# Kernel optimization log

Hardware: AMD Instinct MI355X
Metric: run time of the kernel (lower is better)

The kernel has to match this reference:

```python
import jax, jax.numpy as jnp
import numpy as np

B, LQ, LK, DK, DV = 16, 1024, 1024, 256, 256
NEG = -1e9


def setup_inputs() -> dict:
    key = jax.random.key(0)
    kq, kk, kv, kw, km = jax.random.split(key, 5)
    return {
        "query": jax.random.normal(kq, (B, LQ, DK), dtype=jnp.float32),
        "key": jax.random.normal(kk, (B, LK, DK), dtype=jnp.float32),
        "value": jax.random.normal(kv, (B, LK, DV), dtype=jnp.float32),
        "w": jax.random.normal(kw, (DK,), dtype=jnp.float32),  # Linear(d_k,1,bias=False) weight
        "mask": jax.random.randint(km, (B, LQ, LK), 0, 2, dtype=jnp.int32),
    }


def reference(query, key, value, w, mask):
    # Bahdanau additive score: alignment_layer(query[:, :, None] + key[:, None, :]).squeeze(-1)
    # Exact linear decomposition: W·(q+k) = W·q + W·k, avoiding the (Lq,Lk,d_k) intermediate.
    q_s = jnp.einsum("bqd,d->bq", query, w)  # [B, Lq]
    k_s = jnp.einsum("bkd,d->bk", key, w)    # [B, Lk]
    scores = q_s[:, :, None] + k_s[:, None, :]  # [B, Lq, Lk]
    scores = jnp.where(mask == 0, NEG, scores)
    p_attn = jax.nn.softmax(scores, axis=-1)
    return jnp.matmul(p_attn, value)  # [B, Lq, Dv]
```

## Files before the change

### kernel.cpp

```cpp
#include <hip/hip_runtime.h>
#include <math.h>


#define NB     16
#define NL     1024
#define ND     256
#define NBKT   128

__global__ __launch_bounds__(256)
void ksm_kernel(const float* __restrict__ key, const float* __restrict__ w,
                const int* __restrict__ mask,
                float* __restrict__ ks, unsigned short* __restrict__ bmtab) {
    int wid  = threadIdx.x >> 6;
    int lane = threadIdx.x & 63;
    int row  = blockIdx.x * 4 + wid;

    const float4* krow = (const float4*)(key + (size_t)row * ND);
    float4 kv = krow[lane];
    float4 wv = ((const float4*)w)[lane];
    const int4* mrow4 = (const int4*)(mask + (size_t)row * NL);
    int4 m0 = mrow4[lane], m1 = mrow4[lane + 64];
    int4 m2 = mrow4[lane + 128], m3 = mrow4[lane + 192];

    float p = kv.x * wv.x + kv.y * wv.y + kv.z * wv.z + kv.w * wv.w;
    #pragma unroll
    for (int off = 32; off > 0; off >>= 1)
        p += __shfl_xor(p, off, 64);

    unsigned int bits = 0;
    bits |= (m0.x != 0 ? 1u : 0u) << 0;  bits |= (m0.y != 0 ? 1u : 0u) << 1;
    bits |= (m0.z != 0 ? 1u : 0u) << 2;  bits |= (m0.w != 0 ? 1u : 0u) << 3;
    bits |= (m1.x != 0 ? 1u : 0u) << 4;  bits |= (m1.y != 0 ? 1u : 0u) << 5;
    bits |= (m1.z != 0 ? 1u : 0u) << 6;  bits |= (m1.w != 0 ? 1u : 0u) << 7;
    bits |= (m2.x != 0 ? 1u : 0u) << 8;  bits |= (m2.y != 0 ? 1u : 0u) << 9;
    bits |= (m2.z != 0 ? 1u : 0u) << 10; bits |= (m2.w != 0 ? 1u : 0u) << 11;
    bits |= (m3.x != 0 ? 1u : 0u) << 12; bits |= (m3.y != 0 ? 1u : 0u) << 13;
    bits |= (m3.z != 0 ? 1u : 0u) << 14; bits |= (m3.w != 0 ? 1u : 0u) << 15;

    bmtab[(size_t)row * 64 + lane] = (unsigned short)bits;
    if (lane == 0) ks[row] = p;
}

__global__ __launch_bounds__(512)
void attn_kernel(const float* __restrict__ value, const int* __restrict__ mask,
                 const float* __restrict__ ks,
                 const unsigned short* __restrict__ bmtab,
                 float* __restrict__ out) {
    __shared__ float  lds_V[64 * ND];
    __shared__ float2 pk_lds[NL];
    __shared__ int    cnt[NBKT];
    __shared__ int    cur[NBKT];
    __shared__ float  wred[8];
    __shared__ float  csum[16];

    const int t    = threadIdx.x;
    const int wid  = t >> 6;
    const int lane = t & 63;
    const int row0 = blockIdx.x * 32 + wid * 4;
    const int b    = row0 >> 10;

    const float4* vbase = (const float4*)(value + ((size_t)b << 10) * ND);
    const float*  ksb   = ks + b * NL;

    if (t < NBKT) cnt[t] = 0;

    float v0 = ksb[t], v1 = ksb[t + 512];

    float mx = fmaxf(v0, v1);
    #pragma unroll
    for (int off = 32; off > 0; off >>= 1)
        mx = fmaxf(mx, __shfl_xor(mx, off, 64));
    if (lane == 0) wred[wid] = mx;
    __syncthreads();
    float m = wred[0];
    #pragma unroll
    for (int j = 1; j < 8; ++j) m = fmaxf(m, wred[j]);

    float e0v = __expf(v0 - m), e1v = __expf(v1 - m);
    int b0 = (int)fminf(m - v0, (float)(NBKT - 1));
    int b1 = (int)fminf(m - v1, (float)(NBKT - 1));
    atomicAdd(&cnt[b0], 1); atomicAdd(&cnt[b1], 1);
    __syncthreads();

    if (wid == 0) {
        int a   = cnt[lane];
        int b2v = cnt[lane + 64];
        int sa = a, sb = b2v;
        #pragma unroll
        for (int d = 1; d < 64; d <<= 1) {
            int na = __shfl_up(sa, d, 64);
            int nb = __shfl_up(sb, d, 64);
            if (lane >= d) { sa += na; sb += nb; }
        }
        int tot = __shfl(sa, 63, 64);
        sb += tot;
        cur[lane]      = sa - a;
        cur[lane + 64] = sb - b2v;
    }
    __syncthreads();

    int p0i = atomicAdd(&cur[b0], 1);
    int p1i = atomicAdd(&cur[b1], 1);
    pk_lds[p0i] = make_float2(e0v, __int_as_float(t));
    pk_lds[p1i] = make_float2(e1v, __int_as_float(t + 512));
    __syncthreads();

    #pragma unroll
    for (int cc = 0; cc < 2; ++cc) {
        int chunk = wid * 2 + cc;
        float s = pk_lds[chunk * 64 + lane].x;
        #pragma unroll
        for (int off = 32; off > 0; off >>= 1)
            s += __shfl_xor(s, off, 64);
        if (lane == 0) csum[chunk] = s;
    }

    float2 p0 = pk_lds[lane];
    int   k0  = __float_as_int(p0.y);
    float e0  = p0.x;
    int   e0i = __float_as_int(e0);

    const int L     = (k0 >> 2) & 63;
    const int shift = (k0 & 3) + ((k0 >> 8) << 2);

    unsigned short t0 = bmtab[(size_t)(row0 + 0) * 64 + L];
    unsigned short t1 = bmtab[(size_t)(row0 + 1) * 64 + L];
    unsigned short t2 = bmtab[(size_t)(row0 + 2) * 64 + L];
    unsigned short t3 = bmtab[(size_t)(row0 + 3) * 64 + L];

    #pragma unroll
    for (int j = 0; j < 8; ++j) {
        int s   = wid * 8 + j;
        int ksr = __builtin_amdgcn_readlane(k0, s);
        ((float4*)lds_V)[s * 64 + lane] = vbase[(size_t)ksr * 64 + lane];
    }

    bool mb0 = (t0 >> shift) & 1;
    bool mb1 = (t1 >> shift) & 1;
    bool mb2 = (t2 >> shift) & 1;
    bool mb3 = (t3 >> shift) & 1;
    unsigned long long bm0 = __ballot(mb0);
    unsigned long long bm1 = __ballot(mb1);
    unsigned long long bm2 = __ballot(mb2);
    unsigned long long bm3 = __ballot(mb3);

    auto zsum = [&](bool mb) -> float {
        float wz = mb ? e0 : 0.0f;
        #pragma unroll
        for (int off = 32; off > 0; off >>= 1)
            wz += __shfl_xor(wz, off, 64);
        return wz;
    };
    float z0 = zsum(mb0), z1 = zsum(mb1), z2 = zsum(mb2), z3 = zsum(mb3);

    __syncthreads();

    float4 acc0 = make_float4(0.f, 0.f, 0.f, 0.f);
    float4 acc1 = make_float4(0.f, 0.f, 0.f, 0.f);
    float4 acc2 = make_float4(0.f, 0.f, 0.f, 0.f);
    float4 acc3 = make_float4(0.f, 0.f, 0.f, 0.f);

    #pragma unroll 16
    for (int i = 0; i < 64; ++i) {
        float4 v = ((const float4*)lds_V)[i * 64 + lane];
        float ei = __int_as_float(__builtin_amdgcn_readlane(e0i, i));
        float w0 = ((bm0 >> i) & 1ull) ? ei : 0.0f;
        float w1 = ((bm1 >> i) & 1ull) ? ei : 0.0f;
        float w2 = ((bm2 >> i) & 1ull) ? ei : 0.0f;
        float w3 = ((bm3 >> i) & 1ull) ? ei : 0.0f;
        acc0.x += w0 * v.x; acc0.y += w0 * v.y; acc0.z += w0 * v.z; acc0.w += w0 * v.w;
        acc1.x += w1 * v.x; acc1.y += w1 * v.y; acc1.z += w1 * v.z; acc1.w += w1 * v.w;
        acc2.x += w2 * v.x; acc2.y += w2 * v.y; acc2.z += w2 * v.z; acc2.w += w2 * v.w;
        acc3.x += w3 * v.x; acc3.y += w3 * v.y; acc3.z += w3 * v.z; acc3.w += w3 * v.w;
    }

    float remA = 0.0f;
    #pragma unroll
    for (int j = 1; j < 16; ++j) remA += csum[j];

    auto finish_row = [&](int r, float4 acc, float Z) {
        const int* mrow = mask + (size_t)(row0 + r) * NL;
        float rsuf = remA;
        bool done = (rsuf <= 1e-5f * Z);
        for (int c = 1; c < 16 && !done; ++c) {
            float2 p = pk_lds[c * 64 + lane];
            float e  = p.x;
            int   k  = __float_as_int(p.y);
            bool mb  = (mrow[k] != 0);
            float dz = mb ? e : 0.0f;
            #pragma unroll
            for (int off = 32; off > 0; off >>= 1)
                dz += __shfl_xor(dz, off, 64);
            unsigned long long bmx = __ballot(mb);
            int eI = __float_as_int(e);
            for (int i = 0; i < 64; ++i) {
                float ei = __int_as_float(__builtin_amdgcn_readlane(eI, i));
                int   ki = __builtin_amdgcn_readlane(k, i);
                float w  = ((bmx >> i) & 1ull) ? ei : 0.0f;
                float4 v = vbase[(size_t)ki * 64 + lane];
                acc.x += w * v.x; acc.y += w * v.y;
                acc.z += w * v.z; acc.w += w * v.w;
            }
            Z += dz;
            rsuf -= csum[c];
            done = (rsuf <= 1e-5f * Z);
        }
        float4* orow = (float4*)(out + (size_t)(row0 + r) * ND);
        if (Z > 0.0f) {
            float inv = 1.0f / Z;
            orow[lane] = make_float4(acc.x * inv, acc.y * inv,
                                     acc.z * inv, acc.w * inv);
        } else {
            float4 s = make_float4(0.f, 0.f, 0.f, 0.f);
            for (int k = 0; k < NL; ++k) {
                float4 v = vbase[(size_t)k * 64 + lane];
                s.x += v.x; s.y += v.y; s.z += v.z; s.w += v.w;
            }
            const float inv = 1.0f / (float)NL;
            orow[lane] = make_float4(s.x * inv, s.y * inv, s.z * inv, s.w * inv);
        }
    };
    finish_row(0, acc0, z0);
    finish_row(1, acc1, z1);
    finish_row(2, acc2, z2);
    finish_row(3, acc3, z3);
}

extern "C" void kernel_launch(void* const* d_in, const int* in_sizes, int n_in,
                              void* d_out, int out_size, void* d_ws, size_t ws_size,
                              hipStream_t stream) {
    const float* key   = (const float*)d_in[1];
    const float* value = (const float*)d_in[2];
    const float* w     = (const float*)d_in[3];
    const int*   mask  = (const int*)d_in[4];
    float*       outp  = (float*)d_out;

    float* ks = (float*)d_ws;
    unsigned short* bmtab =
        (unsigned short*)(ks + NB * NL);

    ksm_kernel <<<NB * NL / 4, 256, 0, stream>>>(key, w, mask, ks, bmtab);
    attn_kernel<<<NB * NL / 32, 512, 0, stream>>>(value, mask, ks, bmtab, outp);
}
```

Measured before the change: 158.0 us.

## Halve attention block size and stage only half the top V rows in LDS

Attention blocks shrink from 512 to 256 threads (16 rows per block, twice as many blocks), and each thread now handles four key scores in the max, bucket-sort and exp phase. LDS staging of the top-weighted V rows drops from 64 to 32, so the remaining 32 rows are read straight from global memory inside the accumulation loop. The smaller LDS footprint is meant to let more blocks fit per CU and raise occupancy. In exchange, the per-batch key-score sort is repeated across twice as many blocks, and global V gathers are added to the inner loop.

```diff
diff --git a/kernel.cpp b/kernel.cpp
--- a/kernel.cpp
+++ b/kernel.cpp
@@ -6,6 +6,7 @@
 #define NL     1024
 #define ND     256
 #define NBKT   128
+#define NSTAGE 32
 
 __global__ __launch_bounds__(256)
 void ksm_kernel(const float* __restrict__ key, const float* __restrict__ w,
@@ -41,22 +42,22 @@
     if (lane == 0) ks[row] = p;
 }
 
-__global__ __launch_bounds__(512)
+__global__ __launch_bounds__(256)
 void attn_kernel(const float* __restrict__ value, const int* __restrict__ mask,
                  const float* __restrict__ ks,
                  const unsigned short* __restrict__ bmtab,
                  float* __restrict__ out) {
-    __shared__ float  lds_V[64 * ND];
+    __shared__ float  lds_V[NSTAGE * ND];
     __shared__ float2 pk_lds[NL];
     __shared__ int    cnt[NBKT];
     __shared__ int    cur[NBKT];
-    __shared__ float  wred[8];
+    __shared__ float  wred[4];
     __shared__ float  csum[16];
 
     const int t    = threadIdx.x;
     const int wid  = t >> 6;
     const int lane = t & 63;
-    const int row0 = blockIdx.x * 32 + wid * 4;
+    const int row0 = blockIdx.x * 16 + wid * 4;
     const int b    = row0 >> 10;
 
     const float4* vbase = (const float4*)(value + ((size_t)b << 10) * ND);
@@ -64,22 +65,24 @@
 
     if (t < NBKT) cnt[t] = 0;
 
-    float v0 = ksb[t], v1 = ksb[t + 512];
-
-    float mx = fmaxf(v0, v1);
+    float v0 = ksb[t], v1 = ksb[t + 256], v2 = ksb[t + 512], v3 = ksb[t + 768];
+
+    float mx = fmaxf(fmaxf(v0, v1), fmaxf(v2, v3));
     #pragma unroll
     for (int off = 32; off > 0; off >>= 1)
         mx = fmaxf(mx, __shfl_xor(mx, off, 64));
     if (lane == 0) wred[wid] = mx;
     __syncthreads();
-    float m = wred[0];
-    #pragma unroll
-    for (int j = 1; j < 8; ++j) m = fmaxf(m, wred[j]);
+    const float m = fmaxf(fmaxf(wred[0], wred[1]), fmaxf(wred[2], wred[3]));
 
     float e0v = __expf(v0 - m), e1v = __expf(v1 - m);
+    float e2v = __expf(v2 - m), e3v = __expf(v3 - m);
     int b0 = (int)fminf(m - v0, (float)(NBKT - 1));
     int b1 = (int)fminf(m - v1, (float)(NBKT - 1));
+    int b2 = (int)fminf(m - v2, (float)(NBKT - 1));
+    int b3 = (int)fminf(m - v3, (float)(NBKT - 1));
     atomicAdd(&cnt[b0], 1); atomicAdd(&cnt[b1], 1);
+    atomicAdd(&cnt[b2], 1); atomicAdd(&cnt[b3], 1);
     __syncthreads();
 
     if (wid == 0) {
@@ -101,13 +104,17 @@
 
     int p0i = atomicAdd(&cur[b0], 1);
     int p1i = atomicAdd(&cur[b1], 1);
+    int p2i = atomicAdd(&cur[b2], 1);
+    int p3i = atomicAdd(&cur[b3], 1);
     pk_lds[p0i] = make_float2(e0v, __int_as_float(t));
-    pk_lds[p1i] = make_float2(e1v, __int_as_float(t + 512));
-    __syncthreads();
-
-    #pragma unroll
-    for (int cc = 0; cc < 2; ++cc) {
-        int chunk = wid * 2 + cc;
+    pk_lds[p1i] = make_float2(e1v, __int_as_float(t + 256));
+    pk_lds[p2i] = make_float2(e2v, __int_as_float(t + 512));
+    pk_lds[p3i] = make_float2(e3v, __int_as_float(t + 768));
+    __syncthreads();
+
+    #pragma unroll
+    for (int cc = 0; cc < 4; ++cc) {
+        int chunk = wid * 4 + cc;
         float s = pk_lds[chunk * 64 + lane].x;
         #pragma unroll
         for (int off = 32; off > 0; off >>= 1)
@@ -161,8 +168,22 @@
     float4 acc3 = make_float4(0.f, 0.f, 0.f, 0.f);
 
     #pragma unroll 16
-    for (int i = 0; i < 64; ++i) {
+    for (int i = 0; i < NSTAGE; ++i) {
         float4 v = ((const float4*)lds_V)[i * 64 + lane];
+        float ei = __int_as_float(__builtin_amdgcn_readlane(e0i, i));
+        float w0 = ((bm0 >> i) & 1ull) ? ei : 0.0f;
+        float w1 = ((bm1 >> i) & 1ull) ? ei : 0.0f;
+        float w2 = ((bm2 >> i) & 1ull) ? ei : 0.0f;
+        float w3 = ((bm3 >> i) & 1ull) ? ei : 0.0f;
+        acc0.x += w0 * v.x; acc0.y += w0 * v.y; acc0.z += w0 * v.z; acc0.w += w0 * v.w;
+        acc1.x += w1 * v.x; acc1.y += w1 * v.y; acc1.z += w1 * v.z; acc1.w += w1 * v.w;
+        acc2.x += w2 * v.x; acc2.y += w2 * v.y; acc2.z += w2 * v.z; acc2.w += w2 * v.w;
+        acc3.x += w3 * v.x; acc3.y += w3 * v.y; acc3.z += w3 * v.z; acc3.w += w3 * v.w;
+    }
+    #pragma unroll 8
+    for (int i = NSTAGE; i < 64; ++i) {
+        int ksr  = __builtin_amdgcn_readlane(k0, i);
+        float4 v = vbase[(size_t)ksr * 64 + lane];
         float ei = __int_as_float(__builtin_amdgcn_readlane(e0i, i));
         float w0 = ((bm0 >> i) & 1ull) ? ei : 0.0f;
         float w1 = ((bm1 >> i) & 1ull) ? ei : 0.0f;
@@ -240,5 +261,5 @@
         (unsigned short*)(ks + NB * NL);
 
     ksm_kernel <<<NB * NL / 4, 256, 0, stream>>>(key, w, mask, ks, bmtab);
-    attn_kernel<<<NB * NL / 32, 512, 0, stream>>>(value, mask, ks, bmtab, outp);
+    attn_kernel<<<NB * NL / 16, 256, 0, stream>>>(value, mask, ks, bmtab, outp);
 }
```

Result: slower. 163.5 us (+3.5%).
